# Kernel tuning notes

Measured on AMD Instinct MI355X. Metric: run time of the kernel, lower is better.

The kernel has to match this reference:

```python
import jax, jax.numpy as jnp
import numpy as np

SEQ_LEN = 2048
EMBED = 1024
HIDDEN = 1024
BATCH = 8

def setup_inputs() -> dict:
    key = jax.random.key(0)
    ks = jax.random.split(key, 7)
    scale = (6.0 / (EMBED + HIDDEN)) ** 0.5  # xavier_uniform
    inputs = jax.random.normal(ks[0], (BATCH, SEQ_LEN, EMBED), dtype=jnp.float32)
    Wq = jax.random.uniform(ks[1], (EMBED, HIDDEN), minval=-scale, maxval=scale, dtype=jnp.float32)
    Wk = jax.random.uniform(ks[2], (EMBED, HIDDEN), minval=-scale, maxval=scale, dtype=jnp.float32)
    Wv = jax.random.uniform(ks[3], (EMBED, HIDDEN), minval=-scale, maxval=scale, dtype=jnp.float32)
    bq = jax.random.normal(ks[4], (HIDDEN,), dtype=jnp.float32) * 0.01
    bk = jax.random.normal(ks[5], (HIDDEN,), dtype=jnp.float32) * 0.01
    bv = jax.random.normal(ks[6], (HIDDEN,), dtype=jnp.float32) * 0.01
    return {"inputs": inputs, "Wq": Wq, "bq": bq, "Wk": Wk, "bk": bk, "Wv": Wv, "bv": bv}

def reference(inputs, Wq, bq, Wk, bk, Wv, bv):
    # inputs: [B, S, E]
    q = jnp.einsum('bse,eh->bsh', inputs, Wq) + bq  # [B,S,H]
    k = jnp.einsum('bse,eh->bsh', inputs, Wk) + bk
    v = jnp.einsum('bse,eh->bsh', inputs, Wv) + bv
    scores = jnp.einsum('bqh,bkh->bqk', q, k) / jnp.sqrt(jnp.float32(HIDDEN))  # [B,S,S]
    causal = jnp.tril(jnp.ones((SEQ_LEN, SEQ_LEN), dtype=bool))
    scores = jnp.where(causal, scores, -jnp.inf)
    attn = jax.nn.softmax(scores, axis=-1)
    return jnp.einsum('bqk,bkh->bqh', attn, v)
```

## Files before the change

kernel.cpp:

```cpp
#include <hip/hip_runtime.h>

#define B_ 8
#define S_ 2048
#define E_ 1024
#define H_ 1024

typedef __attribute__((ext_vector_type(8))) short bf16x8;
typedef __attribute__((ext_vector_type(4))) float f32x4;

__device__ inline short f2bf(float f) {
  unsigned u = __builtin_bit_cast(unsigned, f);
  unsigned r = u + 0x7FFFu + ((u >> 16) & 1u);
  return (short)(r >> 16);
}
__device__ inline float bf2f(short s) {
  unsigned u = ((unsigned)(unsigned short)s) << 16;
  return __builtin_bit_cast(float, u);
}

__device__ inline void async16(const void* g, void* l) {
  __builtin_amdgcn_global_load_lds((const __attribute__((address_space(1))) void*)g,
                                   (__attribute__((address_space(3))) void*)l,
                                   16, 0, 0);
}

__global__ __launch_bounds__(256)
void cvt_f32_bf16(const float* __restrict__ in, short* __restrict__ out, int n4) {
  int i = blockIdx.x * blockDim.x + threadIdx.x;
  const int stride = gridDim.x * blockDim.x;
  for (; i < n4; i += stride) {
    float4 v = ((const float4*)in)[i];
    short4 o;
    o.x = f2bf(v.x); o.y = f2bf(v.y); o.z = f2bf(v.z); o.w = f2bf(v.w);
    ((short4*)out)[i] = o;
  }
}

__global__ __launch_bounds__(256)
void transpose_w(const float* __restrict__ W0, const float* __restrict__ W1,
                 const float* __restrict__ W2, short* __restrict__ Wt) {
  const float* W = (blockIdx.z == 0) ? W0 : (blockIdx.z == 1) ? W1 : W2;
  short* out = Wt + (size_t)blockIdx.z * H_ * E_;
  __shared__ __align__(16) float t[64][65];
  const int h0 = blockIdx.x * 64, e0 = blockIdx.y * 64;
  const int r = threadIdx.x >> 4;
  const int c = (threadIdx.x & 15) * 4;
#pragma unroll
  for (int p = 0; p < 4; ++p) {
    int rr = r + p * 16;
    float4 v = *(const float4*)&W[(size_t)(e0 + rr) * H_ + h0 + c];
    t[rr][c + 0] = v.x; t[rr][c + 1] = v.y; t[rr][c + 2] = v.z; t[rr][c + 3] = v.w;
  }
  __syncthreads();
#pragma unroll
  for (int p = 0; p < 4; ++p) {
    int rr = r + p * 16;
    short4 o;
    o.x = f2bf(t[c + 0][rr]); o.y = f2bf(t[c + 1][rr]);
    o.z = f2bf(t[c + 2][rr]); o.w = f2bf(t[c + 3][rr]);
    *(short4*)&out[(size_t)(h0 + rr) * E_ + e0 + c] = o;
  }
}


#define BAR() asm volatile("s_barrier" ::: "memory")
#define VMC(n) asm volatile("s_waitcnt vmcnt(" #n ")" ::: "memory")

#define RD_B(buf, ks)                                                        \
  _Pragma("unroll")                                                          \
  for (int n = 0; n < 4; ++n)                                                \
    bfr[n] = *(const bf16x8*)(lBp + (buf) * 32768 + (ks) * 16384 +           \
                              ((wc * 64 + n * 16 + lr) << 6) + aCol)

#define RD_A(buf, ks, mh)                                                    \
  _Pragma("unroll")                                                          \
  for (int m = 0; m < 4; ++m)                                                \
    af[m] = *(const bf16x8*)(lAp + (buf) * 32768 + (ks) * 16384 +            \
                             ((wr * 128 + (mh) * 64 + m * 16 + lr) << 6) + aCol)

#define MFMA16(mh)                                                           \
  _Pragma("unroll")                                                          \
  for (int m = 0; m < 4; ++m) {                                              \
    _Pragma("unroll")                                                        \
    for (int n = 0; n < 4; ++n)                                              \
      acc[(mh) * 4 + m][n] = __builtin_amdgcn_mfma_f32_16x16x32_bf16(        \
          af[m], bfr[n], acc[(mh) * 4 + m][n], 0, 0, 0);                     \
  }

#define STAGE_A(buf, ks, kt) do {                                            \
    const short* _s = A + (size_t)(m0 + srow) * ldA + (kt) * 64 + (ks) * 32 + scol; \
    char* _d = (char*)lAp + (buf) * 32768 + (ks) * 16384 + wv * 1024;        \
    async16(_s, _d);                                                         \
    async16(_s + (size_t)128 * ldA, _d + 8192);                              \
  } while (0)

#define STAGE_B(buf, ks, kt) do {                                            \
    const short* _s = Bt + (size_t)(n0 + srow) * ldBt + (kt) * 64 + (ks) * 32 + scol; \
    char* _d = (char*)lBp + (buf) * 32768 + (ks) * 16384 + wv * 1024;        \
    async16(_s, _d);                                                         \
    async16(_s + (size_t)128 * ldBt, _d + 8192);                             \
  } while (0)

#define PHASE(buf, ks, mh, STG, WT) do {                                     \
    if ((mh) == 0) { RD_B(buf, ks); }                                        \
    RD_A(buf, ks, mh);                                                       \
    STG;                                                                     \
    WT;                                                                      \
    BAR();                                                                   \
    asm volatile("s_waitcnt lgkmcnt(0)" ::: "memory");                       \
    __builtin_amdgcn_sched_barrier(0);                                       \
    __builtin_amdgcn_s_setprio(1);                                           \
    MFMA16(mh);                                                              \
    __builtin_amdgcn_s_setprio(0);                                           \
    BAR();                                                                   \
  } while (0)

template <int MODE>
__global__ __launch_bounds__(512, 2)
void gemm8(const short* __restrict__ A, const short* __restrict__ Bt,
           void* __restrict__ C0, void* __restrict__ C1, void* __restrict__ C2,
           const float* __restrict__ b0, const float* __restrict__ b1,
           const float* __restrict__ b2,
           float* __restrict__ PlO,
           int K, int ldA, int ldBt, int ldC,
           size_t zsA, size_t zsB, size_t zsC, float scale) {
  int bx, by, z;
  {
    const int bid = blockIdx.x;
    if (MODE == 0) {
      int t = (bid & 7) * 96 + (bid >> 3);
      by = t / 12; bx = t % 12; z = 0;
    } else if (MODE == 1) {
      int t = (bid & 7) * 36 + (bid >> 3);
      z = t / 36;
      int u = t % 36;
      by = 0;
      while (u >= (by + 1) * (by + 2) / 2) ++by;
      bx = u - by * (by + 1) / 2;
    } else {
      int t = (bid & 7) * 32 + (bid >> 3);
      z = t >> 5;
      int rem = t & 31;
      by = rem >> 2; bx = rem & 3;
    }
  }
  A  += (size_t)z * zsA;
  Bt += (size_t)z * zsB;

  __shared__ __align__(16) short lA[2][2][256 * 32];
  __shared__ __align__(16) short lB[2][2][256 * 32];
  __shared__ float sLi[256];
  const char* lAp = (const char*)&lA[0][0][0];
  const char* lBp = (const char*)&lB[0][0][0];

  const int tid = threadIdx.x;
  const int lane = tid & 63;
  const int wv = tid >> 6;
  const int wr = wv >> 2, wc = wv & 3;
  const int lr = lane & 15, kg = lane >> 4;
  const int m0 = by * 256, n0 = bx * 256;
  const int kEnd = (MODE == 2) ? (by + 1) * 256 : K;
  const int nt = kEnd >> 6;
  const int nIter = nt >> 1;

  const int aCol = (kg * 16) ^ ((lr & 8) << 2);
  const int srow = tid >> 2;
  const int scol = (((tid & 3) * 16) ^ (tid & 32)) >> 1;

  if (MODE == 2 && tid < 256) {
    float l = 0.f;
    for (int kt = 0; kt <= by; ++kt)
      l += PlO[((size_t)z * 8 + kt) * S_ + m0 + tid];
    sLi[tid] = 1.f / l;
  }

  f32x4 acc[8][4];
#pragma unroll
  for (int m = 0; m < 8; ++m)
#pragma unroll
    for (int n = 0; n < 4; ++n) acc[m][n] = (f32x4){0.f, 0.f, 0.f, 0.f};
  bf16x8 bfr[4], af[4];

  STAGE_B(0, 0, 0); STAGE_A(0, 0, 0); STAGE_B(0, 1, 0); STAGE_A(0, 1, 0);
  STAGE_B(1, 0, 1); STAGE_A(1, 0, 1); STAGE_B(1, 1, 1);
  VMC(6);
  if (MODE == 2) asm volatile("s_waitcnt lgkmcnt(0)" ::: "memory");
  BAR();

  for (int i = 0; i < nIter; ++i) {
    const int T = 2 * i;
    const bool lastI = (i == nIter - 1);
    PHASE(0, 0, 0, STAGE_A(1, 1, T + 1), (void)0);
    PHASE(0, 0, 1, if (!lastI) { STAGE_B(0, 0, T + 2); }, (void)0);
    PHASE(0, 1, 0, if (!lastI) { STAGE_A(0, 0, T + 2); }, (void)0);
    PHASE(0, 1, 1, if (!lastI) { STAGE_B(0, 1, T + 2); },
          if (lastI) { VMC(0); } else { VMC(6); });
    PHASE(1, 0, 0, if (!lastI) { STAGE_A(0, 1, T + 2); }, (void)0);
    PHASE(1, 0, 1, if (!lastI) { STAGE_B(1, 0, T + 3); }, (void)0);
    PHASE(1, 1, 0, if (!lastI) { STAGE_A(1, 0, T + 3); }, (void)0);
    PHASE(1, 1, 1, if (!lastI) { STAGE_B(1, 1, T + 3); },
          if (!lastI) { VMC(6); });
  }

  if (MODE == 0 && (n0 >> 10) == 2) {
    short* tv = (short*)lAp;
    const int zb = by >> 3;
    const int sb = (by & 7) * 256;
    short* VT = (short*)C2 + (size_t)zb * H_ * S_;
    const int hseg = n0 - 2048;
#pragma unroll
    for (int p = 0; p < 2; ++p) {
      if ((wc >> 1) == p) {
#pragma unroll
        for (int mq = 0; mq < 8; ++mq) {
          int sr = wr * 128 + (mq >> 2) * 64 + (mq & 3) * 16 + kg * 4;
#pragma unroll
          for (int n = 0; n < 4; ++n) {
            int c = wc * 64 + n * 16 + lr;
            float bb = b2[hseg + c];
            f32x4 v = acc[mq][n];
            short4 o;
            o.x = f2bf(v[0] + bb); o.y = f2bf(v[1] + bb);
            o.z = f2bf(v[2] + bb); o.w = f2bf(v[3] + bb);
            *(short4*)&tv[(c & 127) * 264 + sr] = o;
          }
        }
      }
      __syncthreads();
#pragma unroll
      for (int i = 0; i < 8; ++i) {
        int chunk = i * 512 + tid;
        int h = chunk >> 5, sc = (chunk & 31) * 8;
        bf16x8 v8 = *(const bf16x8*)&tv[h * 264 + sc];
        *(bf16x8*)&VT[(size_t)(hseg + p * 128 + h) * S_ + sb + sc] = v8;
      }
      __syncthreads();
    }
    return;
  }
  if (MODE == 1) {
    float* tmpL = (float*)lAp;
    short* C = (short*)C0 + (size_t)z * zsC;
    const bool diag = (bx == by);
#pragma unroll
    for (int mq = 0; mq < 8; ++mq) {
      int rt0 = wr * 128 + (mq >> 2) * 64 + (mq & 3) * 16 + kg * 4;
#pragma unroll
      for (int r = 0; r < 4; ++r) {
        int rt = rt0 + r;
        float se = 0.f;
#pragma unroll
        for (int n = 0; n < 4; ++n) {
          int c = wc * 64 + n * 16 + lr;
          bool ok = !diag || (c <= rt);
          short sh = ok ? f2bf(__expf(acc[mq][n][r] * scale)) : (short)0;
          se += bf2f(sh);
          C[(size_t)(m0 + rt) * ldC + n0 + c] = sh;
        }
#pragma unroll
        for (int o = 1; o < 16; o <<= 1) se += __shfl_xor(se, o);
        if (lr == 0) tmpL[rt * 4 + wc] = se;
      }
    }
    __syncthreads();
    if (tid < 256) {
      float l = tmpL[tid * 4 + 0] + tmpL[tid * 4 + 1] +
                tmpL[tid * 4 + 2] + tmpL[tid * 4 + 3];
      PlO[((size_t)z * 8 + bx) * S_ + m0 + tid] = l;
    }
    return;
  }
#pragma unroll
  for (int mq = 0; mq < 8; ++mq) {
    int rowb = m0 + wr * 128 + (mq >> 2) * 64 + (mq & 3) * 16 + kg * 4;
#pragma unroll
    for (int n = 0; n < 4; ++n) {
      int col = n0 + wc * 64 + n * 16 + lr;
      f32x4 v = acc[mq][n];
      if (MODE == 0) {
        int seg = n0 >> 10;
        const float* bp = (seg == 0) ? b0 : b1;
        short* C = (short*)((seg == 0) ? C0 : C1);
        int cl = col & 1023;
        float bb = bp[cl];
#pragma unroll
        for (int r = 0; r < 4; ++r)
          C[(size_t)(rowb + r) * ldC + cl] = f2bf(v[r] + bb);
      } else {
        float* C = (float*)C0 + (size_t)z * zsC;
        f32x4 liv = *(const f32x4*)&sLi[rowb - m0];
#pragma unroll
        for (int r = 0; r < 4; ++r)
          C[(size_t)(rowb + r) * ldC + col] = v[r] * liv[r];
      }
    }
  }
}

extern "C" void kernel_launch(void* const* d_in, const int* in_sizes, int n_in,
                              void* d_out, int out_size, void* d_ws, size_t ws_size,
                              hipStream_t stream) {
  const float* X  = (const float*)d_in[0];
  const float* Wq = (const float*)d_in[1];
  const float* bq = (const float*)d_in[2];
  const float* Wk = (const float*)d_in[3];
  const float* bk = (const float*)d_in[4];
  const float* Wv = (const float*)d_in[5];
  const float* bv = (const float*)d_in[6];

  char* ws = (char*)d_ws;
  const size_t MB = 1024ull * 1024ull;
  short* Pbuf = (short*)ws;
  short* Xbf  = (short*)ws;
  short* Q    = (short*)(ws + 64 * MB);
  short* Kb   = (short*)(ws + 96 * MB);
  short* Vt   = (short*)(ws + 128 * MB);
  short* Wt   = (short*)(ws + 160 * MB);
  float* Pl   = (float*)(ws + 160 * MB);

  cvt_f32_bf16<<<2048, 256, 0, stream>>>(X, Xbf, (int)((size_t)B_ * S_ * E_ / 4));
  transpose_w<<<dim3(H_ / 64, E_ / 64, 3), 256, 0, stream>>>(Wq, Wk, Wv, Wt);
  gemm8<0><<<768, 512, 0, stream>>>(
      Xbf, Wt, Q, Kb, Vt, bq, bk, bv, nullptr,
      E_, E_, E_, H_, 0, 0, 0, 1.f);
  gemm8<1><<<288, 512, 0, stream>>>(
      Q, Kb, Pbuf, nullptr, nullptr, nullptr, nullptr, nullptr, Pl,
      H_, H_, H_, S_, (size_t)S_ * H_, (size_t)S_ * H_, (size_t)S_ * S_, 0.03125f);
  gemm8<2><<<256, 512, 0, stream>>>(
      Pbuf, Vt, d_out, nullptr, nullptr, nullptr, nullptr, nullptr, Pl,
      S_, S_, S_, H_, (size_t)S_ * S_, (size_t)H_ * S_, (size_t)S_ * H_, 1.f);
}
```

Baseline: 274.7 us.

## Split long causal PV rows into two kernels to balance work

The P·V GEMM for row blocks 4-7 is split along K. The MODE 2 launch now handles only the first 1024 keys for those blocks and writes unnormalized partials. A new MODE 3 launch processes the remaining keys, adds the partial read back from the output and applies the normalization. This caps per-block K length so the longest blocks no longer dominate the tail, at the cost of an extra launch and a read-modify-write of part of the output.

```diff
diff --git a/kernel.cpp b/kernel.cpp
--- a/kernel.cpp
+++ b/kernel.cpp
@@ -137,15 +137,21 @@
       by = 0;
       while (u >= (by + 1) * (by + 2) / 2) ++by;
       bx = u - by * (by + 1) / 2;
-    } else {
+    } else if (MODE == 2) {
       int t = (bid & 7) * 32 + (bid >> 3);
       z = t >> 5;
       int rem = t & 31;
       by = rem >> 2; bx = rem & 3;
+    } else {
+      int t = (bid & 7) * 16 + (bid >> 3);
+      z = t >> 4;
+      int rem = t & 15;
+      by = 4 + (rem >> 2); bx = rem & 3;
     }
   }
   A  += (size_t)z * zsA;
   Bt += (size_t)z * zsB;
+  if (MODE == 3) { A += 1024; Bt += 1024; }
 
   __shared__ __align__(16) short lA[2][2][256 * 32];
   __shared__ __align__(16) short lB[2][2][256 * 32];
@@ -159,7 +165,9 @@
   const int wr = wv >> 2, wc = wv & 3;
   const int lr = lane & 15, kg = lane >> 4;
   const int m0 = by * 256, n0 = bx * 256;
-  const int kEnd = (MODE == 2) ? (by + 1) * 256 : K;
+  const int kEnd = (MODE == 0 || MODE == 1) ? K
+                 : (MODE == 2) ? ((by < 4) ? (by + 1) * 256 : 1024)
+                 : (by + 1) * 256 - 1024;
   const int nt = kEnd >> 6;
   const int nIter = nt >> 1;
 
@@ -167,7 +175,7 @@
   const int srow = tid >> 2;
   const int scol = (((tid & 3) * 16) ^ (tid & 32)) >> 1;
 
-  if (MODE == 2 && tid < 256) {
+  if ((MODE == 2 || MODE == 3) && tid < 256) {
     float l = 0.f;
     for (int kt = 0; kt <= by; ++kt)
       l += PlO[((size_t)z * 8 + kt) * S_ + m0 + tid];
@@ -184,7 +192,7 @@
   STAGE_B(0, 0, 0); STAGE_A(0, 0, 0); STAGE_B(0, 1, 0); STAGE_A(0, 1, 0);
   STAGE_B(1, 0, 1); STAGE_A(1, 0, 1); STAGE_B(1, 1, 1);
   VMC(6);
-  if (MODE == 2) asm volatile("s_waitcnt lgkmcnt(0)" ::: "memory");
+  if (MODE == 2 || MODE == 3) asm volatile("s_waitcnt lgkmcnt(0)" ::: "memory");
   BAR();
 
   for (int i = 0; i < nIter; ++i) {
@@ -286,12 +294,26 @@
 #pragma unroll
         for (int r = 0; r < 4; ++r)
           C[(size_t)(rowb + r) * ldC + cl] = f2bf(v[r] + bb);
+      } else if (MODE == 2) {
+        float* C = (float*)C0 + (size_t)z * zsC;
+        if (by < 4) {
+          f32x4 liv = *(const f32x4*)&sLi[rowb - m0];
+#pragma unroll
+          for (int r = 0; r < 4; ++r)
+            C[(size_t)(rowb + r) * ldC + col] = v[r] * liv[r];
+        } else {
+#pragma unroll
+          for (int r = 0; r < 4; ++r)
+            C[(size_t)(rowb + r) * ldC + col] = v[r];
+        }
       } else {
         float* C = (float*)C0 + (size_t)z * zsC;
         f32x4 liv = *(const f32x4*)&sLi[rowb - m0];
 #pragma unroll
-        for (int r = 0; r < 4; ++r)
-          C[(size_t)(rowb + r) * ldC + col] = v[r] * liv[r];
+        for (int r = 0; r < 4; ++r) {
+          size_t idx = (size_t)(rowb + r) * ldC + col;
+          C[idx] = (C[idx] + v[r]) * liv[r];
+        }
       }
     }
   }
@@ -329,4 +351,7 @@
   gemm8<2><<<256, 512, 0, stream>>>(
       Pbuf, Vt, d_out, nullptr, nullptr, nullptr, nullptr, nullptr, Pl,
       S_, S_, S_, H_, (size_t)S_ * S_, (size_t)H_ * S_, (size_t)S_ * H_, 1.f);
-}
+  gemm8<3><<<128, 512, 0, stream>>>(
+      Pbuf, Vt, d_out, nullptr, nullptr, nullptr, nullptr, nullptr, Pl,
+      S_, S_, S_, H_, (size_t)S_ * S_, (size_t)H_ * S_, (size_t)S_ * H_, 1.f);
+}
```

Measured after the change: 308.1 us. 1.12x slower.
